# Kernel optimization log

Measured on AMD Instinct MI355X. Metric: run time of the kernel, lower is better.

The kernel has to match this reference:

```python
import jax, jax.numpy as jnp
import numpy as np

N = 50000        # nodes
F_IN = 256       # input feature dim
H = 256          # hidden dim
C = 40           # classes
E = 1_600_000    # edges (avg degree 32)
NNZ = 50000      # nonzeros in PvT (one per output row)


def _linear_init(key, fan_in, fan_out):
    k1, k2 = jax.random.split(key)
    bound = 1.0 / np.sqrt(fan_in)
    w = jax.random.uniform(k1, (fan_in, fan_out), jnp.float32, -bound, bound)
    b = jax.random.uniform(k2, (fan_out,), jnp.float32, -bound, bound)
    return w, b


def setup_inputs() -> dict:
    key = jax.random.key(0)
    ks = jax.random.split(key, 8)
    x = jax.random.normal(ks[0], (N, F_IN), jnp.float32)
    edge_src = jax.random.randint(ks[1], (E,), 0, N, jnp.int32)
    edge_dst = jax.random.randint(ks[2], (E,), 0, N, jnp.int32)
    pvt_row = jax.random.randint(ks[3], (NNZ,), 0, N, jnp.int32)
    pvt_col = jax.random.randint(ks[4], (NNZ,), 0, N, jnp.int32)
    pvt_val = jax.random.uniform(ks[5], (NNZ,), jnp.float32)
    w1, b1 = _linear_init(jax.random.fold_in(key, 10), F_IN, H)
    w2, b2 = _linear_init(jax.random.fold_in(key, 11), H, H)
    wfc, bfc = _linear_init(jax.random.fold_in(key, 12), H, C)
    return {"x": x, "edge_src": edge_src, "edge_dst": edge_dst,
            "pvt_row": pvt_row, "pvt_col": pvt_col, "pvt_val": pvt_val,
            "w1": w1, "b1": b1, "w2": w2, "b2": b2, "wfc": wfc, "bfc": bfc}


def _mpnn_conv(x, w, b, src, dst):
    # message: relu(linear(x_j)) per edge; aggregate: scatter-add at dst
    msg = jax.nn.relu(x[src] @ w + b)               # [E', out]
    return jax.ops.segment_sum(msg, dst, num_segments=N)


def reference(x, edge_src, edge_dst, pvt_row, pvt_col, pvt_val,
              w1, b1, w2, b2, wfc, bfc):
    # add self loops (done once per conv in torch, identical edge set here)
    loops = jnp.arange(N, dtype=edge_src.dtype)
    src = jnp.concatenate([edge_src, loops])
    dst = jnp.concatenate([edge_dst, loops])

    h = _mpnn_conv(x, w1, b1, src, dst)
    h = jax.nn.relu(h)            # dropout p=0.5 is identity in eval mode
    h = _mpnn_conv(h, w2, b2, src, dst)
    h = jax.nn.relu(h)
    h = h @ wfc + bfc             # [N, C]
    # sparse PvT @ h via gather-scale-scatter
    h = jax.ops.segment_sum(pvt_val[:, None] * h[pvt_col], pvt_row,
                            num_segments=N)
    return jax.nn.log_softmax(h, axis=1)
```

## Files before the change

### kernel.cpp

```cpp
#include <hip/hip_runtime.h>
#include <hip/hip_bf16.h>
#include <math.h>


#define F_DIM 256
#define C_DIM 40
#define NBUCK 256
#define NB    256
#define MAXCHUNK 6400
#define CAP   16384

typedef _Float16 half8 __attribute__((ext_vector_type(8)));
typedef _Float16 h2    __attribute__((ext_vector_type(2)));
typedef float    f32x4 __attribute__((ext_vector_type(4)));

__device__ __forceinline__ void fp8x4_acc(unsigned w, h2& alo, h2& ahi)
{
    const unsigned lo = (w << 7) & 0x3f803f80u;
    const unsigned hi = (w >> 1) & 0x3f803f80u;
    alo += __builtin_bit_cast(h2, lo);
    ahi += __builtin_bit_cast(h2, hi);
}

__device__ __forceinline__ unsigned q8(float v)
{
    const unsigned short hb = __builtin_bit_cast(unsigned short, (_Float16)v);
    int t = ((hb + 0x40) >> 7) - 64;
    t = t < 0 ? 0 : (t > 126 ? 126 : t);
    return (unsigned)t;
}

__global__ __launch_bounds__(256) void cvt_w1(
    const float* __restrict__ w1, _Float16* __restrict__ w1t)
{
    const int k = blockIdx.x, n = threadIdx.x;
    w1t[n * 256 + k] = (_Float16)w1[k * 256 + n];
}

template <bool AF32>
__device__ __forceinline__ void gemm_body(
    char* smemRaw, const void* __restrict__ Av, const _Float16* __restrict__ Wt,
    const float* __restrict__ bias, unsigned char* __restrict__ out, int M, int bid)
{
    constexpr int K = 256;
    constexpr int LDB = 264;
    _Float16* Bs = (_Float16*)smemRaw;

    const int tid  = threadIdx.x;
    const int wave = tid >> 6;
    const int lane = tid & 63;
    const int quad = lane >> 4;
    const int l16  = lane & 15;
    const int row0 = bid * 128;

    const int gr0 = min(row0 + wave * 32 + l16,      M - 1);
    const int gr1 = min(row0 + wave * 32 + 16 + l16, M - 1);

    half8 aReg[2][8];
    if constexpr (AF32) {
        const float* A = (const float*)Av;
        #pragma unroll
        for (int mi = 0; mi < 2; ++mi) {
            const int gr = mi ? gr1 : gr0;
            #pragma unroll
            for (int kk = 0; kk < 8; ++kk) {
                const float4 u0 = *(const float4*)(A + (size_t)gr * K + kk * 32 + quad * 8);
                const float4 u1 = *(const float4*)(A + (size_t)gr * K + kk * 32 + quad * 8 + 4);
                aReg[mi][kk][0] = (_Float16)u0.x; aReg[mi][kk][1] = (_Float16)u0.y;
                aReg[mi][kk][2] = (_Float16)u0.z; aReg[mi][kk][3] = (_Float16)u0.w;
                aReg[mi][kk][4] = (_Float16)u1.x; aReg[mi][kk][5] = (_Float16)u1.y;
                aReg[mi][kk][6] = (_Float16)u1.z; aReg[mi][kk][7] = (_Float16)u1.w;
            }
        }
    } else {
        const _Float16* A = (const _Float16*)Av;
        #pragma unroll
        for (int mi = 0; mi < 2; ++mi) {
            const int gr = mi ? gr1 : gr0;
            #pragma unroll
            for (int kk = 0; kk < 8; ++kk)
                aReg[mi][kk] = *(const half8*)(A + (size_t)gr * K + kk * 32 + quad * 8);
        }
    }

    f32x4 acc[2][16] = {};

    #pragma unroll
    for (int hf = 0; hf < 2; ++hf) {
        if (hf) __syncthreads();
        #pragma unroll
        for (int c = 0; c < 16; ++c) {
            const int idx = c * 256 + tid;
            const int n   = idx >> 5;
            const int ko  = (idx & 31) * 8;
            *(half8*)&Bs[n * LDB + ko] =
                *(const half8*)(Wt + (size_t)(hf * 128 + n) * K + ko);
        }
        __syncthreads();

        #pragma unroll
        for (int kk = 0; kk < 8; ++kk) {
            #pragma unroll
            for (int ni = 0; ni < 8; ++ni) {
                const half8 bf = *(const half8*)&Bs[(ni * 16 + l16) * LDB + kk * 32 + quad * 8];
                acc[0][hf * 8 + ni] = __builtin_amdgcn_mfma_f32_16x16x32_f16(
                    aReg[0][kk], bf, acc[0][hf * 8 + ni], 0, 0, 0);
                acc[1][hf * 8 + ni] = __builtin_amdgcn_mfma_f32_16x16x32_f16(
                    aReg[1][kk], bf, acc[1][hf * 8 + ni], 0, 0, 0);
            }
        }
    }

    float bv[16];
    #pragma unroll
    for (int ci = 0; ci < 16; ++ci) bv[ci] = bias[ci * 16 + l16];

    #pragma unroll
    for (int mi = 0; mi < 2; ++mi) {
        #pragma unroll
        for (int r = 0; r < 4; ++r) {
            const int grow = row0 + wave * 32 + mi * 16 + quad * 4 + r;
            if (grow < M) {
                uint4 pk;
                unsigned pw[4];
                #pragma unroll
                for (int w = 0; w < 4; ++w) {
                    const int c0 = w * 4;
                    const unsigned b0 = q8(fmaxf(acc[mi][c0 + 0][r] + bv[c0 + 0], 0.f));
                    const unsigned b1 = q8(fmaxf(acc[mi][c0 + 2][r] + bv[c0 + 2], 0.f));
                    const unsigned b2 = q8(fmaxf(acc[mi][c0 + 1][r] + bv[c0 + 1], 0.f));
                    const unsigned b3 = q8(fmaxf(acc[mi][c0 + 3][r] + bv[c0 + 3], 0.f));
                    pw[w] = b0 | (b1 << 8) | (b2 << 16) | (b3 << 24);
                }
                pk.x = pw[0]; pk.y = pw[1]; pk.z = pw[2]; pk.w = pw[3];
                *(uint4*)(out + (size_t)grow * 256 + l16 * 16) = pk;
            }
        }
    }
}

__device__ __forceinline__ void scatter_body(
    char* smemRaw, const int* __restrict__ src, const int* __restrict__ dst,
    int* __restrict__ gcur, int* __restrict__ packed, int E, int chunk, int kblk)
{
    int* lcnt   = (int*)smemRaw;
    int* loff   = lcnt + 256;
    int* cursor = loff + 256;
    int* gbase  = cursor + 256;
    int* segSum = gbase + 256;
    int* ldsOut = segSum + 16;

    const int tid  = threadIdx.x;
    const int wave = tid >> 6;
    const int lane = tid & 63;
    const int e0 = kblk * chunk;
    const int e1 = min(e0 + chunk, E);

    lcnt[tid] = 0;
    __syncthreads();
    for (int i = e0 + tid; i < e1; i += 256)
        atomicAdd(&lcnt[dst[i] >> 8], 1);
    __syncthreads();

    const int v = lcnt[tid];
    {
        int s = v;
        #pragma unroll
        for (int off = 1; off < 64; off <<= 1) {
            const int t = __shfl_up(s, off, 64);
            if (lane >= off) s += t;
        }
        loff[tid] = s - v;
        if (lane == 63) segSum[wave] = s;
    }
    __syncthreads();
    if (tid == 0) {
        int c = 0;
        #pragma unroll
        for (int w = 0; w < 4; ++w) { const int t = segSum[w]; segSum[w] = c; c += t; }
    }
    __syncthreads();
    loff[tid] += segSum[wave];
    gbase[tid] = atomicAdd(&gcur[tid], v);
    cursor[tid] = 0;
    __syncthreads();

    for (int i = e0 + tid; i < e1; i += 256) {
        const int d = dst[i];
        const int b = d >> 8;
        const int pos = atomicAdd(&cursor[b], 1);
        ldsOut[loff[b] + pos] = (src[i] << 8) | (d & 255);
    }
    __syncthreads();

    for (int b = wave; b < NBUCK; b += 4) {
        const int cnt = lcnt[b];
        const int gb  = b * CAP + gbase[b];
        const int lb  = loff[b];
        for (int j = lane; j < cnt; j += 64)
            packed[gb + j] = ldsOut[lb + j];
    }
}

__global__ __launch_bounds__(256, 2) void fused1(
    const float* __restrict__ x, const _Float16* __restrict__ w1t,
    const float* __restrict__ b1, unsigned char* __restrict__ bufM, int M,
    const int* __restrict__ edge_src, const int* __restrict__ edge_dst,
    int* __restrict__ gcur, int* __restrict__ packed, int E, int chunk,
    const float* __restrict__ w2, _Float16* __restrict__ w2t,
    const float* __restrict__ wfc, _Float16* __restrict__ wfcT,
    int gemmBlocks)
{
    __shared__ __align__(16) char smem[128 * 264 * 2];
    const int bid = blockIdx.x;
    if (bid < gemmBlocks) {
        gemm_body<true>(smem, x, w1t, b1, bufM, M, bid);
    } else if (bid < gemmBlocks + NB) {
        scatter_body(smem, edge_src, edge_dst, gcur, packed, E, chunk,
                     bid - gemmBlocks);
    } else {
        const int r = bid - gemmBlocks - NB;
        const int n = threadIdx.x;
        if (r < 256) {
            const int tr = ((r & 15) << 4) | (r >> 4);
            w2t[n * 256 + r] = (_Float16)w2[tr * 256 + n];
        } else {
            const int k  = r - 256;
            const int tk = ((k & 15) << 4) | (k >> 4);
            if (n < 48)
                wfcT[n * 256 + k] = (n < C_DIM) ? (_Float16)wfc[tk * C_DIM + n]
                                                : (_Float16)0.f;
        }
    }
}

__global__ __launch_bounds__(256, 2) void gemm_l2(
    const _Float16* __restrict__ A, const _Float16* __restrict__ Wt,
    const float* __restrict__ bias, unsigned char* __restrict__ out, int M)
{
    __shared__ __align__(16) char smem[128 * 264 * 2];
    gemm_body<false>(smem, A, Wt, bias, out, M, blockIdx.x);
}

__global__ __launch_bounds__(256) void bucket_to_csr(
    const int* __restrict__ packed, const int* __restrict__ gcur,
    int* __restrict__ rowptr, int* __restrict__ rowEnd,
    int* __restrict__ csr_src, int N)
{
    __shared__ int lcnt[NBUCK], loff[NBUCK], cursor[NBUCK], gscan[NBUCK];
    __shared__ int segSum[4];
    const int tid  = threadIdx.x;
    const int wave = tid >> 6;
    const int lane = tid & 63;
    const int b    = blockIdx.x;
    const int nodeBase = b * NBUCK;
    if (nodeBase >= N) return;

    {
        const int v = gcur[tid];
        int s = v;
        #pragma unroll
        for (int off = 1; off < 64; off <<= 1) {
            const int t = __shfl_up(s, off, 64);
            if (lane >= off) s += t;
        }
        if (lane == 63) segSum[wave] = s;
        gscan[tid] = s - v;
    }
    __syncthreads();
    if (tid == 0) {
        int c = 0;
        #pragma unroll
        for (int w = 0; w < 4; ++w) { const int t = segSum[w]; segSum[w] = c; c += t; }
    }
    __syncthreads();
    gscan[tid] += segSum[wave];
    __syncthreads();
    const int cbase = gscan[b];
    const int cnt   = gcur[b];
    const int pbeg  = b * CAP;

    lcnt[tid] = 0;
    __syncthreads();

    for (int e = tid; e < cnt; e += 256)
        atomicAdd(&lcnt[packed[pbeg + e] & 255], 1);
    __syncthreads();

    {
        const int v = lcnt[tid];
        int s = v;
        #pragma unroll
        for (int off = 1; off < 64; off <<= 1) {
            const int t = __shfl_up(s, off, 64);
            if (lane >= off) s += t;
        }
        loff[tid] = s - v;
        if (lane == 63) segSum[wave] = s;
    }
    __syncthreads();
    if (tid == 0) {
        int c = 0;
        #pragma unroll
        for (int w = 0; w < 4; ++w) { const int t = segSum[w]; segSum[w] = c; c += t; }
    }
    __syncthreads();
    loff[tid] += segSum[wave];
    cursor[tid] = 0;
    __syncthreads();

    if (nodeBase + tid < N) {
        rowptr[nodeBase + tid] = cbase + loff[tid];
        rowEnd[nodeBase + tid] = cbase + loff[tid] + lcnt[tid];
    }
    __syncthreads();

    for (int e = tid; e < cnt; e += 256) {
        const int p = packed[pbeg + e];
        const int node = p & 255;
        const int pos = atomicAdd(&cursor[node], 1);
        csr_src[cbase + loff[node] + pos] = p >> 8;
    }
}

__device__ __forceinline__ void gather_core(
    const unsigned char* __restrict__ msgS, const int* __restrict__ csr_src,
    int beg, int end, int rl, int gsrc,
    h2& a0, h2& a1, h2& a2, h2& a3)
{
    int sv = (beg + rl < end) ? csr_src[beg + rl] : 0;
    for (int e0 = beg; e0 < end; e0 += 32) {
        const int n = min(32, end - e0);
        int svn = 0;
        if (e0 + 32 < end)
            svn = (e0 + 32 + rl < end) ? csr_src[e0 + 32 + rl] : 0;
        int j = 0;
        for (; j + 16 <= n; j += 16) {
            int s[16];
            #pragma unroll
            for (int u = 0; u < 16; ++u) s[u] = __shfl(sv, gsrc + j + u, 64);
            uint2 v[16];
            #pragma unroll
            for (int u = 0; u < 16; ++u)
                v[u] = *(const uint2*)(msgS + (size_t)s[u] * F_DIM);
            #pragma unroll
            for (int u = 0; u < 16; ++u) {
                fp8x4_acc(v[u].x, a0, a1);
                fp8x4_acc(v[u].y, a2, a3);
            }
        }
        for (; j + 8 <= n; j += 8) {
            int s[8];
            #pragma unroll
            for (int u = 0; u < 8; ++u) s[u] = __shfl(sv, gsrc + j + u, 64);
            uint2 v[8];
            #pragma unroll
            for (int u = 0; u < 8; ++u)
                v[u] = *(const uint2*)(msgS + (size_t)s[u] * F_DIM);
            #pragma unroll
            for (int u = 0; u < 8; ++u) {
                fp8x4_acc(v[u].x, a0, a1);
                fp8x4_acc(v[u].y, a2, a3);
            }
        }
        for (; j < n; ++j) {
            const int s = __shfl(sv, gsrc + j, 64);
            const uint2 w = *(const uint2*)(msgS + (size_t)s * F_DIM);
            fp8x4_acc(w.x, a0, a1);
            fp8x4_acc(w.y, a2, a3);
        }
        sv = svn;
    }
}

__global__ __launch_bounds__(512) void csr_gather_fp8(
    const unsigned char* __restrict__ msg, const int* __restrict__ rowptr,
    const int* __restrict__ rowEnd, const int* __restrict__ csr_src,
    _Float16* __restrict__ h, int N)
{
    const int tid  = threadIdx.x;
    const int wave = tid >> 6;
    const int lane = tid & 63;
    const int g    = lane >> 5;
    const int rl   = lane & 31;
    const int gsrc = lane & 32;
    const int row  = (blockIdx.x * 8 + wave) * 2 + g;
    if (row >= N) return;

    const unsigned char* msgS = msg + rl * 8;
    h2 a0 = {}, a1 = {}, a2 = {}, a3 = {};
    const uint2 w = *(const uint2*)(msgS + (size_t)row * F_DIM);
    fp8x4_acc(w.x, a0, a1);
    fp8x4_acc(w.y, a2, a3);

    gather_core(msgS, csr_src, rowptr[row], rowEnd[row], rl, gsrc, a0, a1, a2, a3);

    const h2 s2 = {(_Float16)256.f, (_Float16)256.f};
    a0 *= s2; a1 *= s2; a2 *= s2; a3 *= s2;
    half8 o;
    o[0] = a0[0]; o[1] = a0[1]; o[2] = a1[0]; o[3] = a1[1];
    o[4] = a2[0]; o[5] = a2[1]; o[6] = a3[0]; o[7] = a3[1];
    *(half8*)(h + (size_t)row * F_DIM + rl * 8) = o;
}

__global__ __launch_bounds__(512) void gather_fc(
    const unsigned char* __restrict__ msg, const int* __restrict__ rowptr,
    const int* __restrict__ rowEnd, const int* __restrict__ csr_src,
    const _Float16* __restrict__ wfcT, const float* __restrict__ bfc,
    float* __restrict__ logits, int N)
{
    constexpr int LDB = 264;
    __shared__ _Float16 Bs[48 * LDB];
    __shared__ _Float16 hs[16 * LDB];

    const int tid  = threadIdx.x;
    const int wave = tid >> 6;
    const int lane = tid & 63;
    const int g    = lane >> 5;
    const int rl   = lane & 31;
    const int gsrc = lane & 32;
    const int row  = blockIdx.x * 16 + wave * 2 + g;

    #pragma unroll
    for (int c = 0; c < 3; ++c) {
        const int idx = c * 512 + tid;
        const int n   = idx >> 5;
        const int ko  = (idx & 31) * 8;
        *(half8*)&Bs[n * LDB + ko] = *(const half8*)(wfcT + (size_t)n * 256 + ko);
    }

    if (row < N) {
        const unsigned char* msgS = msg + rl * 8;
        h2 a0 = {}, a1 = {}, a2 = {}, a3 = {};
        const uint2 w = *(const uint2*)(msgS + (size_t)row * F_DIM);
        fp8x4_acc(w.x, a0, a1);
        fp8x4_acc(w.y, a2, a3);

        gather_core(msgS, csr_src, rowptr[row], rowEnd[row], rl, gsrc,
                    a0, a1, a2, a3);

        const h2 s2 = {(_Float16)256.f, (_Float16)256.f};
        a0 *= s2; a1 *= s2; a2 *= s2; a3 *= s2;
        half8 o;
        o[0] = a0[0]; o[1] = a0[1]; o[2] = a1[0]; o[3] = a1[1];
        o[4] = a2[0]; o[5] = a2[1]; o[6] = a3[0]; o[7] = a3[1];
        *(half8*)&hs[(wave * 2 + g) * LDB + rl * 8] = o;
    }
    __syncthreads();

    if (wave < 3) {
        const int quad = lane >> 4;
        const int l16  = lane & 15;
        const int ni   = wave;
        f32x4 acc = {};
        #pragma unroll
        for (int kk = 0; kk < 8; ++kk) {
            const half8 af = *(const half8*)&hs[l16 * LDB + kk * 32 + quad * 8];
            const half8 bf = *(const half8*)&Bs[(ni * 16 + l16) * LDB + kk * 32 + quad * 8];
            acc = __builtin_amdgcn_mfma_f32_16x16x32_f16(af, bf, acc, 0, 0, 0);
        }
        const int col = ni * 16 + l16;
        if (col < C_DIM) {
            const float b = bfc[col];
            #pragma unroll
            for (int r = 0; r < 4; ++r) {
                const int grow = blockIdx.x * 16 + quad * 4 + r;
                if (grow < N)
                    logits[(size_t)grow * C_DIM + col] = acc[r] + b;
            }
        }
    }
}

__global__ __launch_bounds__(256) void pvt_scatter(
    const float* __restrict__ logits, const int* __restrict__ prow,
    const int* __restrict__ pcol, const float* __restrict__ pval,
    float* __restrict__ out, int nnz)
{
    const int i    = (blockIdx.x * 256 + threadIdx.x) >> 6;
    const int lane = threadIdx.x & 63;
    if (i >= nnz || lane >= C_DIM) return;
    const int r = prow[i];
    const int c = pcol[i];
    const float v = pval[i];
    atomicAdd(out + (size_t)r * C_DIM + lane, v * logits[(size_t)c * C_DIM + lane]);
}

__global__ __launch_bounds__(256) void log_softmax40(float* __restrict__ out, int M)
{
    const int row  = (blockIdx.x * 256 + threadIdx.x) >> 6;
    const int lane = threadIdx.x & 63;
    if (row >= M) return;
    const float v = (lane < C_DIM) ? out[(size_t)row * C_DIM + lane] : -INFINITY;
    float m = v;
    #pragma unroll
    for (int off = 32; off >= 1; off >>= 1)
        m = fmaxf(m, __shfl_xor(m, off, 64));
    float e = (lane < C_DIM) ? expf(v - m) : 0.f;
    float s = e;
    #pragma unroll
    for (int off = 32; off >= 1; off >>= 1)
        s += __shfl_xor(s, off, 64);
    if (lane < C_DIM)
        out[(size_t)row * C_DIM + lane] = v - m - logf(s);
}

extern "C" void kernel_launch(void* const* d_in, const int* in_sizes, int n_in,
                              void* d_out, int out_size, void* d_ws, size_t ws_size,
                              hipStream_t stream)
{
    const float* x        = (const float*)d_in[0];
    const int*   edge_src = (const int*)d_in[1];
    const int*   edge_dst = (const int*)d_in[2];
    const int*   pvt_row  = (const int*)d_in[3];
    const int*   pvt_col  = (const int*)d_in[4];
    const float* pvt_val  = (const float*)d_in[5];
    const float* w1       = (const float*)d_in[6];
    const float* b1       = (const float*)d_in[7];
    const float* w2       = (const float*)d_in[8];
    const float* b2       = (const float*)d_in[9];
    const float* wfc      = (const float*)d_in[10];
    const float* bfc      = (const float*)d_in[11];

    const int N   = in_sizes[0] / F_DIM;
    const int E   = in_sizes[1];
    const int NNZ = in_sizes[3];

    float* out = (float*)d_out;

    const size_t nodeElems = (size_t)N * F_DIM;
    _Float16* w1t     = (_Float16*)d_ws;
    _Float16* w2t     = w1t + 65536;
    _Float16* wfcT    = w2t + 65536;
    unsigned char* bufM = (unsigned char*)(wfcT + 48 * 256);
    _Float16* bufH    = (_Float16*)(bufM + nodeElems);
    float*    logits  = (float*)(bufH + nodeElems);
    int*      gcur    = (int*)(logits + (size_t)N * C_DIM);
    int*      rowptr  = gcur + 256;
    int*      rowEnd  = rowptr + N + 8;
    int*      csr_src = rowEnd + N + 8;
    int*      packed  = (int*)bufH;

    const int chunk = (E + NB - 1) / NB;

    const int gemmBlocks  = (N + 127) / 128;
    const int rowBlocks   = (N + 3) / 4;
    const int gatherBlocks= (N + 15) / 16;
    const int nnzBlocks   = (NNZ + 3) / 4;

    hipMemsetAsync(gcur, 0, 256 * sizeof(int), stream);
    hipMemsetAsync(d_out, 0, (size_t)N * C_DIM * sizeof(float), stream);

    cvt_w1<<<256, 256, 0, stream>>>(w1, w1t);

    fused1<<<gemmBlocks + NB + 512, 256, 0, stream>>>(
        x, w1t, b1, bufM, N, edge_src, edge_dst, gcur, packed, E, chunk,
        w2, w2t, wfc, wfcT, gemmBlocks);

    bucket_to_csr<<<NBUCK, 256, 0, stream>>>(packed, gcur,
                                             rowptr, rowEnd, csr_src, N);

    csr_gather_fp8<<<gatherBlocks, 512, 0, stream>>>(bufM, rowptr, rowEnd,
                                                     csr_src, bufH, N);

    gemm_l2<<<gemmBlocks, 256, 0, stream>>>(bufH, w2t, b2, bufM, N);

    gather_fc<<<gatherBlocks, 512, 0, stream>>>(bufM, rowptr, rowEnd, csr_src,
                                                wfcT, bfc, logits, N);

    pvt_scatter<<<nnzBlocks, 256, 0, stream>>>(logits, pvt_row, pvt_col, pvt_val, out, NNZ);
    log_softmax40<<<rowBlocks, 256, 0, stream>>>(out, N);
}
```

Baseline: 355.7 us.

## Store aggregated layer-1 features as 8-bit and decode in layer-2 GEMM

```diff
diff --git a/kernel.cpp b/kernel.cpp
--- a/kernel.cpp
+++ b/kernel.cpp
@@ -37,7 +37,7 @@
     w1t[n * 256 + k] = (_Float16)w1[k * 256 + n];
 }
 
-template <bool AF32>
+template <int AMODE>
 __device__ __forceinline__ void gemm_body(
     char* smemRaw, const void* __restrict__ Av, const _Float16* __restrict__ Wt,
     const float* __restrict__ bias, unsigned char* __restrict__ out, int M, int bid)
@@ -57,7 +57,7 @@
     const int gr1 = min(row0 + wave * 32 + 16 + l16, M - 1);
 
     half8 aReg[2][8];
-    if constexpr (AF32) {
+    if constexpr (AMODE == 0) {
         const float* A = (const float*)Av;
         #pragma unroll
         for (int mi = 0; mi < 2; ++mi) {
@@ -73,13 +73,22 @@
             }
         }
     } else {
-        const _Float16* A = (const _Float16*)Av;
+        const unsigned char* A = (const unsigned char*)Av;
         #pragma unroll
         for (int mi = 0; mi < 2; ++mi) {
             const int gr = mi ? gr1 : gr0;
             #pragma unroll
-            for (int kk = 0; kk < 8; ++kk)
-                aReg[mi][kk] = *(const half8*)(A + (size_t)gr * K + kk * 32 + quad * 8);
+            for (int kk = 0; kk < 8; ++kk) {
+                const uint2 w = *(const uint2*)(A + (size_t)gr * 256 + kk * 32 + quad * 8);
+                const h2 p01 = __builtin_bit_cast(h2, (w.x << 7) & 0x3f803f80u);
+                const h2 p23 = __builtin_bit_cast(h2, (w.x >> 1) & 0x3f803f80u);
+                const h2 p45 = __builtin_bit_cast(h2, (w.y << 7) & 0x3f803f80u);
+                const h2 p67 = __builtin_bit_cast(h2, (w.y >> 1) & 0x3f803f80u);
+                half8 a;
+                a[0] = p01[0]; a[1] = p01[1]; a[2] = p23[0]; a[3] = p23[1];
+                a[4] = p45[0]; a[5] = p45[1]; a[6] = p67[0]; a[7] = p67[1];
+                aReg[mi][kk] = a;
+            }
         }
     }
 
@@ -114,6 +123,8 @@
     float bv[16];
     #pragma unroll
     for (int ci = 0; ci < 16; ++ci) bv[ci] = bias[ci * 16 + l16];
+
+    constexpr float S = (AMODE == 1) ? 256.f : 1.f;
 
     #pragma unroll
     for (int mi = 0; mi < 2; ++mi) {
@@ -126,10 +137,10 @@
                 #pragma unroll
                 for (int w = 0; w < 4; ++w) {
                     const int c0 = w * 4;
-                    const unsigned b0 = q8(fmaxf(acc[mi][c0 + 0][r] + bv[c0 + 0], 0.f));
-                    const unsigned b1 = q8(fmaxf(acc[mi][c0 + 2][r] + bv[c0 + 2], 0.f));
-                    const unsigned b2 = q8(fmaxf(acc[mi][c0 + 1][r] + bv[c0 + 1], 0.f));
-                    const unsigned b3 = q8(fmaxf(acc[mi][c0 + 3][r] + bv[c0 + 3], 0.f));
+                    const unsigned b0 = q8(fmaxf(fmaf(acc[mi][c0 + 0][r], S, bv[c0 + 0]), 0.f));
+                    const unsigned b1 = q8(fmaxf(fmaf(acc[mi][c0 + 2][r], S, bv[c0 + 2]), 0.f));
+                    const unsigned b2 = q8(fmaxf(fmaf(acc[mi][c0 + 1][r], S, bv[c0 + 1]), 0.f));
+                    const unsigned b3 = q8(fmaxf(fmaf(acc[mi][c0 + 3][r], S, bv[c0 + 3]), 0.f));
                     pw[w] = b0 | (b1 << 8) | (b2 << 16) | (b3 << 24);
                 }
                 pk.x = pw[0]; pk.y = pw[1]; pk.z = pw[2]; pk.w = pw[3];
@@ -214,7 +225,7 @@
     __shared__ __align__(16) char smem[128 * 264 * 2];
     const int bid = blockIdx.x;
     if (bid < gemmBlocks) {
-        gemm_body<true>(smem, x, w1t, b1, bufM, M, bid);
+        gemm_body<0>(smem, x, w1t, b1, bufM, M, bid);
     } else if (bid < gemmBlocks + NB) {
         scatter_body(smem, edge_src, edge_dst, gcur, packed, E, chunk,
                      bid - gemmBlocks);
@@ -235,11 +246,11 @@
 }
 
 __global__ __launch_bounds__(256, 2) void gemm_l2(
-    const _Float16* __restrict__ A, const _Float16* __restrict__ Wt,
+    const unsigned char* __restrict__ A, const _Float16* __restrict__ Wt,
     const float* __restrict__ bias, unsigned char* __restrict__ out, int M)
 {
     __shared__ __align__(16) char smem[128 * 264 * 2];
-    gemm_body<false>(smem, A, Wt, bias, out, M, blockIdx.x);
+    gemm_body<1>(smem, A, Wt, bias, out, M, blockIdx.x);
 }
 
 __global__ __launch_bounds__(256) void bucket_to_csr(
@@ -373,10 +384,10 @@
     }
 }
 
-__global__ __launch_bounds__(512) void csr_gather_fp8(
+__global__ __launch_bounds__(256) void csr_gather_fp8(
     const unsigned char* __restrict__ msg, const int* __restrict__ rowptr,
     const int* __restrict__ rowEnd, const int* __restrict__ csr_src,
-    _Float16* __restrict__ h, int N)
+    unsigned char* __restrict__ h8, int N)
 {
     const int tid  = threadIdx.x;
     const int wave = tid >> 6;
@@ -384,7 +395,7 @@
     const int g    = lane >> 5;
     const int rl   = lane & 31;
     const int gsrc = lane & 32;
-    const int row  = (blockIdx.x * 8 + wave) * 2 + g;
+    const int row  = (blockIdx.x * 4 + wave) * 2 + g;
     if (row >= N) return;
 
     const unsigned char* msgS = msg + rl * 8;
@@ -395,12 +406,13 @@
 
     gather_core(msgS, csr_src, rowptr[row], rowEnd[row], rl, gsrc, a0, a1, a2, a3);
 
-    const h2 s2 = {(_Float16)256.f, (_Float16)256.f};
-    a0 *= s2; a1 *= s2; a2 *= s2; a3 *= s2;
-    half8 o;
-    o[0] = a0[0]; o[1] = a0[1]; o[2] = a1[0]; o[3] = a1[1];
-    o[4] = a2[0]; o[5] = a2[1]; o[6] = a3[0]; o[7] = a3[1];
-    *(half8*)(h + (size_t)row * F_DIM + rl * 8) = o;
+    const float s = 256.f;
+    const unsigned w0 = q8((float)a0[0] * s) | (q8((float)a1[0] * s) << 8) |
+                        (q8((float)a0[1] * s) << 16) | (q8((float)a1[1] * s) << 24);
+    const unsigned w1 = q8((float)a2[0] * s) | (q8((float)a3[0] * s) << 8) |
+                        (q8((float)a2[1] * s) << 16) | (q8((float)a3[1] * s) << 24);
+    uint2 o2; o2.x = w0; o2.y = w1;
+    *(uint2*)(h8 + (size_t)row * 256 + rl * 8) = o2;
 }
 
 __global__ __launch_bounds__(512) void gather_fc(
@@ -410,7 +422,6 @@
     float* __restrict__ logits, int N)
 {
     constexpr int LDB = 264;
-    __shared__ _Float16 Bs[48 * LDB];
     __shared__ _Float16 hs[16 * LDB];
 
     const int tid  = threadIdx.x;
@@ -421,14 +432,6 @@
     const int gsrc = lane & 32;
     const int row  = blockIdx.x * 16 + wave * 2 + g;
 
-    #pragma unroll
-    for (int c = 0; c < 3; ++c) {
-        const int idx = c * 512 + tid;
-        const int n   = idx >> 5;
-        const int ko  = (idx & 31) * 8;
-        *(half8*)&Bs[n * LDB + ko] = *(const half8*)(wfcT + (size_t)n * 256 + ko);
-    }
-
     if (row < N) {
         const unsigned char* msgS = msg + rl * 8;
         h2 a0 = {}, a1 = {}, a2 = {}, a3 = {};
@@ -456,7 +459,7 @@
         #pragma unroll
         for (int kk = 0; kk < 8; ++kk) {
             const half8 af = *(const half8*)&hs[l16 * LDB + kk * 32 + quad * 8];
-            const half8 bf = *(const half8*)&Bs[(ni * 16 + l16) * LDB + kk * 32 + quad * 8];
+            const half8 bf = *(const half8*)(wfcT + (size_t)(ni * 16 + l16) * 256 + kk * 32 + quad * 8);
             acc = __builtin_amdgcn_mfma_f32_16x16x32_f16(af, bf, acc, 0, 0, 0);
         }
         const int col = ni * 16 + l16;
@@ -528,25 +531,26 @@
 
     float* out = (float*)d_out;
 
-    const size_t nodeElems = (size_t)N * F_DIM;
+    const size_t nodeBytes = (size_t)N * F_DIM;
     _Float16* w1t     = (_Float16*)d_ws;
     _Float16* w2t     = w1t + 65536;
     _Float16* wfcT    = w2t + 65536;
     unsigned char* bufM = (unsigned char*)(wfcT + 48 * 256);
-    _Float16* bufH    = (_Float16*)(bufM + nodeElems);
-    float*    logits  = (float*)(bufH + nodeElems);
+    unsigned char* bufH = bufM + nodeBytes;
+    float*    logits  = (float*)(bufH + nodeBytes);
     int*      gcur    = (int*)(logits + (size_t)N * C_DIM);
     int*      rowptr  = gcur + 256;
     int*      rowEnd  = rowptr + N + 8;
     int*      csr_src = rowEnd + N + 8;
-    int*      packed  = (int*)bufH;
+    int*      packed  = csr_src + E;
 
     const int chunk = (E + NB - 1) / NB;
 
-    const int gemmBlocks  = (N + 127) / 128;
-    const int rowBlocks   = (N + 3) / 4;
-    const int gatherBlocks= (N + 15) / 16;
-    const int nnzBlocks   = (NNZ + 3) / 4;
+    const int gemmBlocks   = (N + 127) / 128;
+    const int rowBlocks    = (N + 3) / 4;
+    const int gather1Blocks= (N + 7) / 8;
+    const int gatherFcBlocks = (N + 15) / 16;
+    const int nnzBlocks    = (NNZ + 3) / 4;
 
     hipMemsetAsync(gcur, 0, 256 * sizeof(int), stream);
     hipMemsetAsync(d_out, 0, (size_t)N * C_DIM * sizeof(float), stream);
@@ -560,13 +564,13 @@
     bucket_to_csr<<<NBUCK, 256, 0, stream>>>(packed, gcur,
                                              rowptr, rowEnd, csr_src, N);
 
-    csr_gather_fp8<<<gatherBlocks, 512, 0, stream>>>(bufM, rowptr, rowEnd,
-                                                     csr_src, bufH, N);
+    csr_gather_fp8<<<gather1Blocks, 256, 0, stream>>>(bufM, rowptr, rowEnd,
+                                                      csr_src, bufH, N);
 
     gemm_l2<<<gemmBlocks, 256, 0, stream>>>(bufH, w2t, b2, bufM, N);
 
-    gather_fc<<<gatherBlocks, 512, 0, stream>>>(bufM, rowptr, rowEnd, csr_src,
-                                                wfcT, bfc, logits, N);
+    gather_fc<<<gatherFcBlocks, 512, 0, stream>>>(bufM, rowptr, rowEnd, csr_src,
+                                                  wfcT, bfc, logits, N);
 
     pvt_scatter<<<nnzBlocks, 256, 0, stream>>>(logits, pvt_row, pvt_col, pvt_val, out, NNZ);
     log_softmax40<<<rowBlocks, 256, 0, stream>>>(out, N);
```

After: 356.6 us. About the same (+0.2%).

## Fuse layer-1 gather with layer-2 GEMM and read weights from global

Applied to the files above, without the earlier changes.

```diff
diff --git a/kernel.cpp b/kernel.cpp
--- a/kernel.cpp
+++ b/kernel.cpp
@@ -37,9 +37,8 @@
     w1t[n * 256 + k] = (_Float16)w1[k * 256 + n];
 }
 
-template <bool AF32>
 __device__ __forceinline__ void gemm_body(
-    char* smemRaw, const void* __restrict__ Av, const _Float16* __restrict__ Wt,
+    char* smemRaw, const float* __restrict__ A, const _Float16* __restrict__ Wt,
     const float* __restrict__ bias, unsigned char* __restrict__ out, int M, int bid)
 {
     constexpr int K = 256;
@@ -57,29 +56,17 @@
     const int gr1 = min(row0 + wave * 32 + 16 + l16, M - 1);
 
     half8 aReg[2][8];
-    if constexpr (AF32) {
-        const float* A = (const float*)Av;
-        #pragma unroll
-        for (int mi = 0; mi < 2; ++mi) {
-            const int gr = mi ? gr1 : gr0;
-            #pragma unroll
-            for (int kk = 0; kk < 8; ++kk) {
-                const float4 u0 = *(const float4*)(A + (size_t)gr * K + kk * 32 + quad * 8);
-                const float4 u1 = *(const float4*)(A + (size_t)gr * K + kk * 32 + quad * 8 + 4);
-                aReg[mi][kk][0] = (_Float16)u0.x; aReg[mi][kk][1] = (_Float16)u0.y;
-                aReg[mi][kk][2] = (_Float16)u0.z; aReg[mi][kk][3] = (_Float16)u0.w;
-                aReg[mi][kk][4] = (_Float16)u1.x; aReg[mi][kk][5] = (_Float16)u1.y;
-                aReg[mi][kk][6] = (_Float16)u1.z; aReg[mi][kk][7] = (_Float16)u1.w;
-            }
-        }
-    } else {
-        const _Float16* A = (const _Float16*)Av;
-        #pragma unroll
-        for (int mi = 0; mi < 2; ++mi) {
-            const int gr = mi ? gr1 : gr0;
-            #pragma unroll
-            for (int kk = 0; kk < 8; ++kk)
-                aReg[mi][kk] = *(const half8*)(A + (size_t)gr * K + kk * 32 + quad * 8);
+    #pragma unroll
+    for (int mi = 0; mi < 2; ++mi) {
+        const int gr = mi ? gr1 : gr0;
+        #pragma unroll
+        for (int kk = 0; kk < 8; ++kk) {
+            const float4 u0 = *(const float4*)(A + (size_t)gr * K + kk * 32 + quad * 8);
+            const float4 u1 = *(const float4*)(A + (size_t)gr * K + kk * 32 + quad * 8 + 4);
+            aReg[mi][kk][0] = (_Float16)u0.x; aReg[mi][kk][1] = (_Float16)u0.y;
+            aReg[mi][kk][2] = (_Float16)u0.z; aReg[mi][kk][3] = (_Float16)u0.w;
+            aReg[mi][kk][4] = (_Float16)u1.x; aReg[mi][kk][5] = (_Float16)u1.y;
+            aReg[mi][kk][6] = (_Float16)u1.z; aReg[mi][kk][7] = (_Float16)u1.w;
         }
     }
 
@@ -214,7 +201,7 @@
     __shared__ __align__(16) char smem[128 * 264 * 2];
     const int bid = blockIdx.x;
     if (bid < gemmBlocks) {
-        gemm_body<true>(smem, x, w1t, b1, bufM, M, bid);
+        gemm_body(smem, x, w1t, b1, bufM, M, bid);
     } else if (bid < gemmBlocks + NB) {
         scatter_body(smem, edge_src, edge_dst, gcur, packed, E, chunk,
                      bid - gemmBlocks);
@@ -234,14 +221,6 @@
     }
 }
 
-__global__ __launch_bounds__(256, 2) void gemm_l2(
-    const _Float16* __restrict__ A, const _Float16* __restrict__ Wt,
-    const float* __restrict__ bias, unsigned char* __restrict__ out, int M)
-{
-    __shared__ __align__(16) char smem[128 * 264 * 2];
-    gemm_body<false>(smem, A, Wt, bias, out, M, blockIdx.x);
-}
-
 __global__ __launch_bounds__(256) void bucket_to_csr(
     const int* __restrict__ packed, const int* __restrict__ gcur,
     int* __restrict__ rowptr, int* __restrict__ rowEnd,
@@ -373,45 +352,15 @@
     }
 }
 
-__global__ __launch_bounds__(512) void csr_gather_fp8(
+__global__ __launch_bounds__(512) void gather_gemm_l2(
     const unsigned char* __restrict__ msg, const int* __restrict__ rowptr,
     const int* __restrict__ rowEnd, const int* __restrict__ csr_src,
-    _Float16* __restrict__ h, int N)
-{
-    const int tid  = threadIdx.x;
-    const int wave = tid >> 6;
-    const int lane = tid & 63;
-    const int g    = lane >> 5;
-    const int rl   = lane & 31;
-    const int gsrc = lane & 32;
-    const int row  = (blockIdx.x * 8 + wave) * 2 + g;
-    if (row >= N) return;
-
-    const unsigned char* msgS = msg + rl * 8;
-    h2 a0 = {}, a1 = {}, a2 = {}, a3 = {};
-    const uint2 w = *(const uint2*)(msgS + (size_t)row * F_DIM);
-    fp8x4_acc(w.x, a0, a1);
-    fp8x4_acc(w.y, a2, a3);
-
-    gather_core(msgS, csr_src, rowptr[row], rowEnd[row], rl, gsrc, a0, a1, a2, a3);
-
-    const h2 s2 = {(_Float16)256.f, (_Float16)256.f};
-    a0 *= s2; a1 *= s2; a2 *= s2; a3 *= s2;
-    half8 o;
-    o[0] = a0[0]; o[1] = a0[1]; o[2] = a1[0]; o[3] = a1[1];
-    o[4] = a2[0]; o[5] = a2[1]; o[6] = a3[0]; o[7] = a3[1];
-    *(half8*)(h + (size_t)row * F_DIM + rl * 8) = o;
-}
-
-__global__ __launch_bounds__(512) void gather_fc(
-    const unsigned char* __restrict__ msg, const int* __restrict__ rowptr,
-    const int* __restrict__ rowEnd, const int* __restrict__ csr_src,
-    const _Float16* __restrict__ wfcT, const float* __restrict__ bfc,
-    float* __restrict__ logits, int N)
+    const _Float16* __restrict__ w2t, const float* __restrict__ b2,
+    unsigned char* __restrict__ out, int N)
 {
     constexpr int LDB = 264;
-    __shared__ _Float16 Bs[48 * LDB];
     __shared__ _Float16 hs[16 * LDB];
+    __shared__ unsigned char outT[16 * 256];
 
     const int tid  = threadIdx.x;
     const int wave = tid >> 6;
@@ -421,14 +370,6 @@
     const int gsrc = lane & 32;
     const int row  = blockIdx.x * 16 + wave * 2 + g;
 
-    #pragma unroll
-    for (int c = 0; c < 3; ++c) {
-        const int idx = c * 512 + tid;
-        const int n   = idx >> 5;
-        const int ko  = (idx & 31) * 8;
-        *(half8*)&Bs[n * LDB + ko] = *(const half8*)(wfcT + (size_t)n * 256 + ko);
-    }
-
     if (row < N) {
         const unsigned char* msgS = msg + rl * 8;
         h2 a0 = {}, a1 = {}, a2 = {}, a3 = {};
@@ -439,6 +380,74 @@
         gather_core(msgS, csr_src, rowptr[row], rowEnd[row], rl, gsrc,
                     a0, a1, a2, a3);
 
+        half8 o;
+        o[0] = a0[0]; o[1] = a0[1]; o[2] = a1[0]; o[3] = a1[1];
+        o[4] = a2[0]; o[5] = a2[1]; o[6] = a3[0]; o[7] = a3[1];
+        *(half8*)&hs[(wave * 2 + g) * LDB + rl * 8] = o;
+    }
+    __syncthreads();
+
+    const int quad = lane >> 4;
+    const int l16  = lane & 15;
+    #pragma unroll
+    for (int t = 0; t < 2; ++t) {
+        const int ni = wave * 2 + t;
+        f32x4 acc = {};
+        #pragma unroll
+        for (int kk = 0; kk < 8; ++kk) {
+            const half8 af = *(const half8*)&hs[l16 * LDB + kk * 32 + quad * 8];
+            const half8 bf = *(const half8*)(w2t + (size_t)(ni * 16 + l16) * 256 + kk * 32 + quad * 8);
+            acc = __builtin_amdgcn_mfma_f32_16x16x32_f16(af, bf, acc, 0, 0, 0);
+        }
+        const int c    = ni * 16 + l16;
+        const float bv = b2[c];
+        const int pos  = ((ni & 1) << 1) | ((ni >> 1) & 1);
+        const int boff = l16 * 16 + ((ni >> 2) << 2) + pos;
+        #pragma unroll
+        for (int r = 0; r < 4; ++r) {
+            const float v = fmaxf(fmaf(acc[r], 256.f, bv), 0.f);
+            outT[(quad * 4 + r) * 256 + boff] = (unsigned char)q8(v);
+        }
+    }
+    __syncthreads();
+
+    if (tid < 256) {
+        const int r    = tid >> 4;
+        const int seg  = tid & 15;
+        const int grow = blockIdx.x * 16 + r;
+        if (grow < N)
+            *(uint4*)(out + (size_t)grow * 256 + seg * 16) =
+                *(const uint4*)&outT[r * 256 + seg * 16];
+    }
+}
+
+__global__ __launch_bounds__(512) void gather_fc(
+    const unsigned char* __restrict__ msg, const int* __restrict__ rowptr,
+    const int* __restrict__ rowEnd, const int* __restrict__ csr_src,
+    const _Float16* __restrict__ wfcT, const float* __restrict__ bfc,
+    float* __restrict__ logits, int N)
+{
+    constexpr int LDB = 264;
+    __shared__ _Float16 hs[16 * LDB];
+
+    const int tid  = threadIdx.x;
+    const int wave = tid >> 6;
+    const int lane = tid & 63;
+    const int g    = lane >> 5;
+    const int rl   = lane & 31;
+    const int gsrc = lane & 32;
+    const int row  = blockIdx.x * 16 + wave * 2 + g;
+
+    if (row < N) {
+        const unsigned char* msgS = msg + rl * 8;
+        h2 a0 = {}, a1 = {}, a2 = {}, a3 = {};
+        const uint2 w = *(const uint2*)(msgS + (size_t)row * F_DIM);
+        fp8x4_acc(w.x, a0, a1);
+        fp8x4_acc(w.y, a2, a3);
+
+        gather_core(msgS, csr_src, rowptr[row], rowEnd[row], rl, gsrc,
+                    a0, a1, a2, a3);
+
         const h2 s2 = {(_Float16)256.f, (_Float16)256.f};
         a0 *= s2; a1 *= s2; a2 *= s2; a3 *= s2;
         half8 o;
@@ -456,7 +465,7 @@
         #pragma unroll
         for (int kk = 0; kk < 8; ++kk) {
             const half8 af = *(const half8*)&hs[l16 * LDB + kk * 32 + quad * 8];
-            const half8 bf = *(const half8*)&Bs[(ni * 16 + l16) * LDB + kk * 32 + quad * 8];
+            const half8 bf = *(const half8*)(wfcT + (size_t)(ni * 16 + l16) * 256 + kk * 32 + quad * 8);
             acc = __builtin_amdgcn_mfma_f32_16x16x32_f16(af, bf, acc, 0, 0, 0);
         }
         const int col = ni * 16 + l16;
@@ -528,25 +537,25 @@
 
     float* out = (float*)d_out;
 
-    const size_t nodeElems = (size_t)N * F_DIM;
+    const size_t nodeBytes = (size_t)N * F_DIM;
     _Float16* w1t     = (_Float16*)d_ws;
     _Float16* w2t     = w1t + 65536;
     _Float16* wfcT    = w2t + 65536;
-    unsigned char* bufM = (unsigned char*)(wfcT + 48 * 256);
-    _Float16* bufH    = (_Float16*)(bufM + nodeElems);
-    float*    logits  = (float*)(bufH + nodeElems);
+    unsigned char* bufM  = (unsigned char*)(wfcT + 48 * 256);
+    unsigned char* bufM2 = bufM + nodeBytes;
+    float*    logits  = (float*)(bufM2 + nodeBytes);
     int*      gcur    = (int*)(logits + (size_t)N * C_DIM);
     int*      rowptr  = gcur + 256;
     int*      rowEnd  = rowptr + N + 8;
     int*      csr_src = rowEnd + N + 8;
-    int*      packed  = (int*)bufH;
+    int*      packed  = csr_src + E;
 
     const int chunk = (E + NB - 1) / NB;
 
-    const int gemmBlocks  = (N + 127) / 128;
-    const int rowBlocks   = (N + 3) / 4;
-    const int gatherBlocks= (N + 15) / 16;
-    const int nnzBlocks   = (NNZ + 3) / 4;
+    const int gemmBlocks   = (N + 127) / 128;
+    const int rowBlocks    = (N + 3) / 4;
+    const int tileBlocks   = (N + 15) / 16;
+    const int nnzBlocks    = (NNZ + 3) / 4;
 
     hipMemsetAsync(gcur, 0, 256 * sizeof(int), stream);
     hipMemsetAsync(d_out, 0, (size_t)N * C_DIM * sizeof(float), stream);
@@ -560,13 +569,11 @@
     bucket_to_csr<<<NBUCK, 256, 0, stream>>>(packed, gcur,
                                              rowptr, rowEnd, csr_src, N);
 
-    csr_gather_fp8<<<gatherBlocks, 512, 0, stream>>>(bufM, rowptr, rowEnd,
-                                                     csr_src, bufH, N);
-
-    gemm_l2<<<gemmBlocks, 256, 0, stream>>>(bufH, w2t, b2, bufM, N);
-
-    gather_fc<<<gatherBlocks, 512, 0, stream>>>(bufM, rowptr, rowEnd, csr_src,
-                                                wfcT, bfc, logits, N);
+    gather_gemm_l2<<<tileBlocks, 512, 0, stream>>>(bufM, rowptr, rowEnd,
+                                                   csr_src, w2t, b2, bufM2, N);
+
+    gather_fc<<<tileBlocks, 512, 0, stream>>>(bufM2, rowptr, rowEnd, csr_src,
+                                              wfcT, bfc, logits, N);
 
     pvt_scatter<<<nnzBlocks, 256, 0, stream>>>(logits, pvt_row, pvt_col, pvt_val, out, NNZ);
     log_softmax40<<<rowBlocks, 256, 0, stream>>>(out, N);
```

After: 385.7 us. 8.4% more time.
